# Performance work log

Hardware: AMD Instinct MI355X
Metric: run time of the kernel (lower is better)

The kernel has to match this reference:

```python
import jax, jax.numpy as jnp
import numpy as np

B, NX, C, KX = 16, 8192, 128, 16  # batch, grid size, channels, retained positive modes


def setup_inputs() -> dict:
    key = jax.random.key(0)
    k1, k2, k3 = jax.random.split(key, 3)
    x = jax.random.normal(k1, (B, NX, C), dtype=jnp.float32)
    scale = 1.0 / (C ** 2)
    w_real = scale * jax.random.uniform(k2, (KX + 1, C, C), dtype=jnp.float32)
    w_imag = scale * jax.random.uniform(k3, (KX + 1, C, C), dtype=jnp.float32)
    return {"x": x, "w_real": w_real, "w_imag": w_imag}


def reference(x, w_real, w_imag):
    # x: (b, nx, c); weights: (kx+1, c, c) complex
    nx = x.shape[1]
    k1 = w_real.shape[0]  # kx + 1 retained frequencies
    w = w_real + 1j * w_imag
    fx = jnp.fft.rfft(x, axis=-2)  # (b, nx//2+1, c) complex
    # torch.matmul(weights, fx[:, :kx+1, :, None])[..., 0]:
    # out[b,k,i] = sum_j w[k,i,j] * fx[b,k,j]
    out_ft = jnp.einsum('kij,bkj->bki', w, fx[:, :k1, :])
    # zero-pad truncated spectrum back to full rfft length, then inverse
    pad = nx // 2 + 1 - k1
    out_full = jnp.pad(out_ft, ((0, 0), (0, pad), (0, 0)))
    return jnp.fft.irfft(out_full, n=nx, axis=-2)
```

## Files before the change

kernel.cpp:

```cpp
#include <hip/hip_runtime.h>
#include <math.h>

#define B_     16
#define NX_    8192
#define C_     128
#define K1_    17
#define KP_    18
#define NC_    64
#define NH_    4096

typedef float v2f __attribute__((ext_vector_type(2)));
typedef float v4f __attribute__((ext_vector_type(4)));

#define GPART_F ((size_t)B_ * K1_ * 2 * NC_ * C_)

__global__ __launch_bounds__(256) void k_fwd(const float* __restrict__ x,
                                             float* __restrict__ ws) {
    __shared__ v4f smem[2 * 64 * 19];

    float* gpart = ws;
    const int b = blockIdx.y;
    const int c = blockIdx.x;
    const int t = threadIdx.x;
    const int jq  = t & 31;
    const int sub = (t >> 5) & 1;
    const int w   = t >> 6;
    const int i0  = c * 64;

    {
        float2* tg = (float2*)smem;
        for (int idx = t; idx < 64 * KP_; idx += 256) {
            int i = idx / KP_;
            int p = idx - i * KP_;
            float2 v = make_float2(0.f, 0.f);
            if (p < K1_) {
                int k = (p < 9) ? 2 * p : 2 * (p - 9) + 1;
                int m = (k * (i0 + i)) & (NX_ - 1);
                float rev = (float)m * (1.0f / (float)NX_);
                v = make_float2(__builtin_amdgcn_cosf(rev),
                                __builtin_amdgcn_sinf(rev));
            }
            tg[idx] = v;
        }
    }
    __syncthreads();

    v4f gr[9], gs[9];
#pragma unroll
    for (int kk = 0; kk < 9; ++kk) { gr[kk] = (v4f)(0.f); gs[kk] = (v4f)(0.f); }

    const size_t xb = (size_t)b * NX_ * C_;
    const int ibase = w * 16;
    const float sg = sub ? -1.f : 1.f;
    const float2* tp = (const float2*)smem + (size_t)ibase * KP_ + sub * 9;
    const float* xlo_p = x + xb + (size_t)(i0 + ibase) * C_ + 4 * jq;
    const float* xhi_p = xlo_p + (size_t)NH_ * C_;

#pragma unroll 4
    for (int s = 0; s < 16; ++s) {
        v4f xlo = *(const v4f*)(xlo_p + (size_t)s * C_);
        v4f xhi = *(const v4f*)(xhi_p + (size_t)s * C_);
        v4f xs = __builtin_elementwise_fma(xhi, (v4f)(sg), xlo);
        const float2* tr = tp + (size_t)s * KP_;
#pragma unroll
        for (int kk = 0; kk < 9; ++kk) {
            float2 tt = tr[kk];
            gr[kk] = __builtin_elementwise_fma(xs, (v4f)(tt.x), gr[kk]);
            gs[kk] = __builtin_elementwise_fma(xs, (v4f)(tt.y), gs[kk]);
        }
    }

    const int lid = t & 63;
    __syncthreads();
    if (w >= 2) {
        v4f* p = smem + ((size_t)(w - 2) * 64 + lid) * 19;
#pragma unroll
        for (int kk = 0; kk < 9; ++kk) { p[2 * kk] = gr[kk]; p[2 * kk + 1] = gs[kk]; }
    }
    __syncthreads();
    if (w < 2) {
        const v4f* p = smem + ((size_t)w * 64 + lid) * 19;
#pragma unroll
        for (int kk = 0; kk < 9; ++kk) { gr[kk] += p[2 * kk]; gs[kk] += p[2 * kk + 1]; }
    }
    __syncthreads();
    if (w == 1) {
        v4f* p = smem + (size_t)lid * 19;
#pragma unroll
        for (int kk = 0; kk < 9; ++kk) { p[2 * kk] = gr[kk]; p[2 * kk + 1] = gs[kk]; }
    }
    __syncthreads();
    if (w == 0) {
        const v4f* p = smem + (size_t)lid * 19;
#pragma unroll
        for (int kk = 0; kk < 9; ++kk) {
            gr[kk] += p[2 * kk];
            gs[kk] += p[2 * kk + 1];
            if (sub == 0 || kk < 8) {
                int k = sub ? 2 * kk + 1 : 2 * kk;
                float* gpR = gpart + ((((size_t)b * K1_ + k) * 2 + 0) * NC_ + c) * C_ + 4 * jq;
                float* gpS = gpart + ((((size_t)b * K1_ + k) * 2 + 1) * NC_ + c) * C_ + 4 * jq;
                *(v4f*)gpR = gr[kk];
                *(v4f*)gpS = gs[kk];
            }
        }
    }
}

__global__ __launch_bounds__(1024) void k_mix(const float* __restrict__ wr_g,
                                              const float* __restrict__ wi_g,
                                              float* __restrict__ ws) {
    const int k = blockIdx.x;
    const int b = blockIdx.y;
    const int t = threadIdx.x;

    const float* gpart = ws;
    float2* acoef = (float2*)(ws + GPART_F);

    __shared__ float part[8][C_];
    __shared__ float gsum[2][C_];
    __shared__ float hp[16][C_];

    {
        const int ch = t & 127, ri = (t >> 7) & 1, sh = t >> 8;
        const float* base = gpart
            + (((size_t)b * K1_ + k) * 2 + ri) * ((size_t)NC_ * C_) + ch;
        float g = 0.f;
#pragma unroll
        for (int s = 0; s < 16; ++s) g += base[(size_t)(sh * 16 + s) * C_];
        part[sh * 2 + ri][ch] = g;
    }
    __syncthreads();
    if (t < 256) {
        const int ch = t & 127, ri = t >> 7;
        gsum[ri][ch] = part[ri][ch] + part[2 + ri][ch]
                     + part[4 + ri][ch] + part[6 + ri][ch];
    }
    __syncthreads();

    {
        const int i = t & 127, q = t >> 7;
        float hr = 0.f, hi = 0.f;
        const float* wrp = wr_g + ((size_t)k * C_ + i) * C_;
        const float* wip = wi_g + ((size_t)k * C_ + i) * C_;
#pragma unroll
        for (int jjj = 0; jjj < 16; ++jjj) {
            int jj = q * 16 + jjj;
            float wr = wrp[jj], wi = wip[jj];
            float a = gsum[0][jj], cc = gsum[1][jj];
            hr = fmaf(wr, a, hr); hr = fmaf( wi, cc, hr);
            hi = fmaf(wi, a, hi); hi = fmaf(-wr, cc, hi);
        }
        hp[q * 2 + 0][i] = hr;
        hp[q * 2 + 1][i] = hi;
    }
    __syncthreads();
    if (t < 128) {
        const int i = t;
        float hr = 0.f, hi = 0.f;
#pragma unroll
        for (int q = 0; q < 8; ++q) { hr += hp[q * 2][i]; hi += hp[q * 2 + 1][i]; }
        float cf = (k == 0 ? 1.0f : 2.0f) / (float)NX_;
        acoef[((size_t)b * K1_ + k) * C_ + i] = make_float2(cf * hr, -cf * hi);
    }
}

__global__ __launch_bounds__(256) void k_inv(float* __restrict__ out,
                                             const float* __restrict__ ws) {
    __shared__ float2 smem[64 * K1_];

    const float4* acoef4 = (const float4*)(ws + GPART_F);
    const int b = blockIdx.y;
    const int c = blockIdx.x;
    const int t = threadIdx.x;
    const int jp = t & 63;
    const int h = t >> 6;
    const int i0 = c * 64;

    for (int idx = t; idx < 64 * K1_; idx += 256) {
        int i = idx / K1_;
        int k = idx - i * K1_;
        int m = (k * (i0 + i)) & (NX_ - 1);
        float rev = (float)m * (1.0f / (float)NX_);
        smem[idx] = make_float2(__builtin_amdgcn_cosf(rev),
                                __builtin_amdgcn_sinf(rev));
    }

    v2f arP[K1_], aiP[K1_];
#pragma unroll
    for (int k = 0; k < K1_; ++k) {
        float4 a = acoef4[((size_t)b * K1_ + k) * (C_ / 2) + jp];
        arP[k] = (v2f){a.x, a.z};
        aiP[k] = (v2f){a.y, a.w};
    }
    __syncthreads();

    const size_t ob = (size_t)b * NX_ * C_;
    const float2* tl = smem + (size_t)h * 16 * K1_;
    float* olo = out + ob + (size_t)(i0 + h * 16) * C_ + 2 * jp;
    float* ohi = olo + (size_t)NH_ * C_;
#pragma unroll 4
    for (int s = 0; s < 16; ++s) {
        const float2* tr = tl + s * K1_;
        v2f Se = (v2f)(0.f), So = (v2f)(0.f);
#pragma unroll
        for (int k = 0; k < K1_; ++k) {
            float2 tt = tr[k];
            v2f cc = {tt.x, tt.x};
            v2f ss = {tt.y, tt.y};
            if ((k & 1) == 0) {
                Se = __builtin_elementwise_fma(arP[k], cc, Se);
                Se = __builtin_elementwise_fma(aiP[k], ss, Se);
            } else {
                So = __builtin_elementwise_fma(arP[k], cc, So);
                So = __builtin_elementwise_fma(aiP[k], ss, So);
            }
        }
        *(v2f*)(olo + (size_t)s * C_) = Se + So;
        *(v2f*)(ohi + (size_t)s * C_) = Se - So;
    }
}

extern "C" void kernel_launch(void* const* d_in, const int* in_sizes, int n_in,
                              void* d_out, int out_size, void* d_ws, size_t ws_size,
                              hipStream_t stream) {
    const float* x  = (const float*)d_in[0];
    const float* wr = (const float*)d_in[1];
    const float* wi = (const float*)d_in[2];
    float* out = (float*)d_out;
    float* ws  = (float*)d_ws;

    k_fwd<<<dim3(NC_, B_), 256, 0, stream>>>(x, ws);
    k_mix<<<dim3(K1_, B_), 1024, 0, stream>>>(wr, wi, ws);
    k_inv<<<dim3(NC_, B_), 256, 0, stream>>>(out, ws);
}
```

Measured before the change: 51.76 us.

## Share twiddle table via workspace between forward and inverse kernels, vectorize twiddle loads

The forward kernel now lays out its twiddle table with an even/odd split padded to 20 entries per row, and the batch-0 blocks write it to workspace. The inverse kernel reads these twiddles from global memory with wave-uniform addresses instead of recomputing cos/sin into LDS and synchronizing. Both kernels now load twiddles as wide float4 vectors and unroll the FMA chains explicitly. The cost is extra global traffic and a dependence on the forward pass having filled the table, which the kernel launch order guarantees within a call.

Result: no change. 51.62 us (-0.3%).

```diff
diff --git a/kernel.cpp b/kernel.cpp
--- a/kernel.cpp
+++ b/kernel.cpp
@@ -5,14 +5,17 @@
 #define NX_    8192
 #define C_     128
 #define K1_    17
-#define KP_    18
+#define QW_    20
 #define NC_    64
 #define NH_    4096
 
 typedef float v2f __attribute__((ext_vector_type(2)));
 typedef float v4f __attribute__((ext_vector_type(4)));
 
-#define GPART_F ((size_t)B_ * K1_ * 2 * NC_ * C_)
+#define GPART_F  ((size_t)B_ * K1_ * 2 * NC_ * C_)
+#define ACOEF_F  ((size_t)B_ * K1_ * C_ * 2)
+#define TRIG_OFF (GPART_F + ACOEF_F)
+
 
 __global__ __launch_bounds__(256) void k_fwd(const float* __restrict__ x,
                                              float* __restrict__ ws) {
@@ -28,19 +31,21 @@
     const int i0  = c * 64;
 
     {
-        float2* tg = (float2*)smem;
-        for (int idx = t; idx < 64 * KP_; idx += 256) {
-            int i = idx / KP_;
-            int p = idx - i * KP_;
+        float2* tg  = (float2*)smem;
+        float2* tgg = (float2*)(ws + TRIG_OFF) + (size_t)c * (64 * QW_);
+        for (int idx = t; idx < 64 * QW_; idx += 256) {
+            int i = idx / QW_;
+            int q = idx - i * QW_;
             float2 v = make_float2(0.f, 0.f);
-            if (p < K1_) {
-                int k = (p < 9) ? 2 * p : 2 * (p - 9) + 1;
+            int k = (q < 9) ? (2 * q) : ((q >= 10 && q < 18) ? (2 * (q - 10) + 1) : -1);
+            if (k >= 0) {
                 int m = (k * (i0 + i)) & (NX_ - 1);
                 float rev = (float)m * (1.0f / (float)NX_);
                 v = make_float2(__builtin_amdgcn_cosf(rev),
                                 __builtin_amdgcn_sinf(rev));
             }
             tg[idx] = v;
+            if (b == 0) tgg[idx] = v;
         }
     }
     __syncthreads();
@@ -52,7 +57,7 @@
     const size_t xb = (size_t)b * NX_ * C_;
     const int ibase = w * 16;
     const float sg = sub ? -1.f : 1.f;
-    const float2* tp = (const float2*)smem + (size_t)ibase * KP_ + sub * 9;
+    const float* tp = (const float*)smem + ((size_t)ibase * QW_ + sub * 10) * 2;
     const float* xlo_p = x + xb + (size_t)(i0 + ibase) * C_ + 4 * jq;
     const float* xhi_p = xlo_p + (size_t)NH_ * C_;
 
@@ -61,13 +66,30 @@
         v4f xlo = *(const v4f*)(xlo_p + (size_t)s * C_);
         v4f xhi = *(const v4f*)(xhi_p + (size_t)s * C_);
         v4f xs = __builtin_elementwise_fma(xhi, (v4f)(sg), xlo);
-        const float2* tr = tp + (size_t)s * KP_;
-#pragma unroll
-        for (int kk = 0; kk < 9; ++kk) {
-            float2 tt = tr[kk];
-            gr[kk] = __builtin_elementwise_fma(xs, (v4f)(tt.x), gr[kk]);
-            gs[kk] = __builtin_elementwise_fma(xs, (v4f)(tt.y), gs[kk]);
-        }
+        const float* tr = tp + (size_t)s * (2 * QW_);
+        float4 t0 = *(const float4*)(tr + 0);
+        float4 t1 = *(const float4*)(tr + 4);
+        float4 t2 = *(const float4*)(tr + 8);
+        float4 t3 = *(const float4*)(tr + 12);
+        float2 t4 = *(const float2*)(tr + 16);
+        gr[0] = __builtin_elementwise_fma(xs, (v4f)(t0.x), gr[0]);
+        gs[0] = __builtin_elementwise_fma(xs, (v4f)(t0.y), gs[0]);
+        gr[1] = __builtin_elementwise_fma(xs, (v4f)(t0.z), gr[1]);
+        gs[1] = __builtin_elementwise_fma(xs, (v4f)(t0.w), gs[1]);
+        gr[2] = __builtin_elementwise_fma(xs, (v4f)(t1.x), gr[2]);
+        gs[2] = __builtin_elementwise_fma(xs, (v4f)(t1.y), gs[2]);
+        gr[3] = __builtin_elementwise_fma(xs, (v4f)(t1.z), gr[3]);
+        gs[3] = __builtin_elementwise_fma(xs, (v4f)(t1.w), gs[3]);
+        gr[4] = __builtin_elementwise_fma(xs, (v4f)(t2.x), gr[4]);
+        gs[4] = __builtin_elementwise_fma(xs, (v4f)(t2.y), gs[4]);
+        gr[5] = __builtin_elementwise_fma(xs, (v4f)(t2.z), gr[5]);
+        gs[5] = __builtin_elementwise_fma(xs, (v4f)(t2.w), gs[5]);
+        gr[6] = __builtin_elementwise_fma(xs, (v4f)(t3.x), gr[6]);
+        gs[6] = __builtin_elementwise_fma(xs, (v4f)(t3.y), gs[6]);
+        gr[7] = __builtin_elementwise_fma(xs, (v4f)(t3.z), gr[7]);
+        gs[7] = __builtin_elementwise_fma(xs, (v4f)(t3.w), gs[7]);
+        gr[8] = __builtin_elementwise_fma(xs, (v4f)(t4.x), gr[8]);
+        gs[8] = __builtin_elementwise_fma(xs, (v4f)(t4.y), gs[8]);
     }
 
     const int lid = t & 63;
@@ -167,55 +189,79 @@
 
 __global__ __launch_bounds__(256) void k_inv(float* __restrict__ out,
                                              const float* __restrict__ ws) {
-    __shared__ float2 smem[64 * K1_];
-
     const float4* acoef4 = (const float4*)(ws + GPART_F);
+    const float* trigg = ws + TRIG_OFF;
     const int b = blockIdx.y;
     const int c = blockIdx.x;
     const int t = threadIdx.x;
     const int jp = t & 63;
-    const int h = t >> 6;
+    const int h = __builtin_amdgcn_readfirstlane(t >> 6);
     const int i0 = c * 64;
 
-    for (int idx = t; idx < 64 * K1_; idx += 256) {
-        int i = idx / K1_;
-        int k = idx - i * K1_;
-        int m = (k * (i0 + i)) & (NX_ - 1);
-        float rev = (float)m * (1.0f / (float)NX_);
-        smem[idx] = make_float2(__builtin_amdgcn_cosf(rev),
-                                __builtin_amdgcn_sinf(rev));
-    }
-
-    v2f arP[K1_], aiP[K1_];
-#pragma unroll
-    for (int k = 0; k < K1_; ++k) {
-        float4 a = acoef4[((size_t)b * K1_ + k) * (C_ / 2) + jp];
-        arP[k] = (v2f){a.x, a.z};
-        aiP[k] = (v2f){a.y, a.w};
-    }
-    __syncthreads();
-
+    v2f arE[9], aiE[9], arO[8], aiO[8];
+#pragma unroll
+    for (int q = 0; q < 9; ++q) {
+        float4 a = acoef4[((size_t)b * K1_ + 2 * q) * (C_ / 2) + jp];
+        arE[q] = (v2f){a.x, a.z}; aiE[q] = (v2f){a.y, a.w};
+    }
+#pragma unroll
+    for (int q = 0; q < 8; ++q) {
+        float4 a = acoef4[((size_t)b * K1_ + 2 * q + 1) * (C_ / 2) + jp];
+        arO[q] = (v2f){a.x, a.z}; aiO[q] = (v2f){a.y, a.w};
+    }
+
+    const float* trow = trigg + ((size_t)c * 64 + h * 16) * (2 * QW_);
     const size_t ob = (size_t)b * NX_ * C_;
-    const float2* tl = smem + (size_t)h * 16 * K1_;
     float* olo = out + ob + (size_t)(i0 + h * 16) * C_ + 2 * jp;
     float* ohi = olo + (size_t)NH_ * C_;
+
 #pragma unroll 4
     for (int s = 0; s < 16; ++s) {
-        const float2* tr = tl + s * K1_;
+        const float* tr = trow + (size_t)s * (2 * QW_);
+        float4 e0 = *(const float4*)(tr + 0);
+        float4 e1 = *(const float4*)(tr + 4);
+        float4 e2 = *(const float4*)(tr + 8);
+        float4 e3 = *(const float4*)(tr + 12);
+        float2 e4 = *(const float2*)(tr + 16);
+        float4 o0 = *(const float4*)(tr + 20);
+        float4 o1 = *(const float4*)(tr + 24);
+        float4 o2 = *(const float4*)(tr + 28);
+        float4 o3 = *(const float4*)(tr + 32);
         v2f Se = (v2f)(0.f), So = (v2f)(0.f);
-#pragma unroll
-        for (int k = 0; k < K1_; ++k) {
-            float2 tt = tr[k];
-            v2f cc = {tt.x, tt.x};
-            v2f ss = {tt.y, tt.y};
-            if ((k & 1) == 0) {
-                Se = __builtin_elementwise_fma(arP[k], cc, Se);
-                Se = __builtin_elementwise_fma(aiP[k], ss, Se);
-            } else {
-                So = __builtin_elementwise_fma(arP[k], cc, So);
-                So = __builtin_elementwise_fma(aiP[k], ss, So);
-            }
-        }
+        Se = __builtin_elementwise_fma(arE[0], (v2f)(e0.x), Se);
+        Se = __builtin_elementwise_fma(aiE[0], (v2f)(e0.y), Se);
+        Se = __builtin_elementwise_fma(arE[1], (v2f)(e0.z), Se);
+        Se = __builtin_elementwise_fma(aiE[1], (v2f)(e0.w), Se);
+        Se = __builtin_elementwise_fma(arE[2], (v2f)(e1.x), Se);
+        Se = __builtin_elementwise_fma(aiE[2], (v2f)(e1.y), Se);
+        Se = __builtin_elementwise_fma(arE[3], (v2f)(e1.z), Se);
+        Se = __builtin_elementwise_fma(aiE[3], (v2f)(e1.w), Se);
+        Se = __builtin_elementwise_fma(arE[4], (v2f)(e2.x), Se);
+        Se = __builtin_elementwise_fma(aiE[4], (v2f)(e2.y), Se);
+        Se = __builtin_elementwise_fma(arE[5], (v2f)(e2.z), Se);
+        Se = __builtin_elementwise_fma(aiE[5], (v2f)(e2.w), Se);
+        Se = __builtin_elementwise_fma(arE[6], (v2f)(e3.x), Se);
+        Se = __builtin_elementwise_fma(aiE[6], (v2f)(e3.y), Se);
+        Se = __builtin_elementwise_fma(arE[7], (v2f)(e3.z), Se);
+        Se = __builtin_elementwise_fma(aiE[7], (v2f)(e3.w), Se);
+        Se = __builtin_elementwise_fma(arE[8], (v2f)(e4.x), Se);
+        Se = __builtin_elementwise_fma(aiE[8], (v2f)(e4.y), Se);
+        So = __builtin_elementwise_fma(arO[0], (v2f)(o0.x), So);
+        So = __builtin_elementwise_fma(aiO[0], (v2f)(o0.y), So);
+        So = __builtin_elementwise_fma(arO[1], (v2f)(o0.z), So);
+        So = __builtin_elementwise_fma(aiO[1], (v2f)(o0.w), So);
+        So = __builtin_elementwise_fma(arO[2], (v2f)(o1.x), So);
+        So = __builtin_elementwise_fma(aiO[2], (v2f)(o1.y), So);
+        So = __builtin_elementwise_fma(arO[3], (v2f)(o1.z), So);
+        So = __builtin_elementwise_fma(aiO[3], (v2f)(o1.w), So);
+        So = __builtin_elementwise_fma(arO[4], (v2f)(o2.x), So);
+        So = __builtin_elementwise_fma(aiO[4], (v2f)(o2.y), So);
+        So = __builtin_elementwise_fma(arO[5], (v2f)(o2.z), So);
+        So = __builtin_elementwise_fma(aiO[5], (v2f)(o2.w), So);
+        So = __builtin_elementwise_fma(arO[6], (v2f)(o3.x), So);
+        So = __builtin_elementwise_fma(aiO[6], (v2f)(o3.y), So);
+        So = __builtin_elementwise_fma(arO[7], (v2f)(o3.z), So);
+        So = __builtin_elementwise_fma(aiO[7], (v2f)(o3.w), So);
         *(v2f*)(olo + (size_t)s * C_) = Se + So;
         *(v2f*)(ohi + (size_t)s * C_) = Se - So;
     }
```
